# Kernel tuning notes

Measured on AMD Instinct MI355X. Metric: run time of the kernel, lower is better.

Reference implementation:

```python
import jax, jax.numpy as jnp
import numpy as np

D_MODEL = 1024
N_HEADS = 16
WINDOW = 256
CAUSAL = True


def build_sliding_window_mask(T, window_size, causal=True):
    half = window_size // 2
    i = jnp.arange(T)[:, None]
    j = jnp.arange(T)[None, :]
    attend = jnp.abs(i - j) <= half
    if causal:
        attend = attend & (j <= i)
    return jnp.where(attend, 0.0, -jnp.inf).astype(jnp.float32)  # (T, T)


def setup_inputs() -> dict:
    key = jax.random.key(0)
    kx, kq, kk, kv, ko = jax.random.split(key, 5)
    B, T, D = 2, 2048, D_MODEL
    s = 1.0 / np.sqrt(D)
    return {
        "x": jax.random.normal(kx, (B, T, D), jnp.float32),
        "Wq": jax.random.normal(kq, (D, D), jnp.float32) * s,
        "Wk": jax.random.normal(kk, (D, D), jnp.float32) * s,
        "Wv": jax.random.normal(kv, (D, D), jnp.float32) * s,
        "Wo": jax.random.normal(ko, (D, D), jnp.float32) * s,
    }


def reference(x, Wq, Wk, Wv, Wo):
    B, T, D = x.shape
    H = N_HEADS
    dh = D // H
    # torch nn.Linear: y = x @ W.T
    def proj(W):
        return (x @ W.T).reshape(B, T, H, dh).transpose(0, 2, 1, 3)  # (B,H,T,dh)

    q, k, v = proj(Wq), proj(Wk), proj(Wv)
    scale = jnp.sqrt(jnp.asarray(dh, x.dtype))
    scores = jnp.einsum("bhtd,bhsd->bhts", q, k) / scale  # (B,H,T,T)
    mask = build_sliding_window_mask(T, WINDOW, CAUSAL)
    scores = scores + mask[None, None]
    attn = jax.nn.softmax(scores, axis=-1)
    attn = jnp.nan_to_num(attn, nan=0.0)
    out = jnp.einsum("bhts,bhsd->bhtd", attn, v)  # (B,H,T,dh)
    out = out.transpose(0, 2, 1, 3).reshape(B, T, D)
    return out @ Wo.T
```

## Files before the change

kernel.cpp:

```cpp
#include <hip/hip_runtime.h>
#include <hip/hip_bf16.h>

#define B_  2
#define T_  2048
#define D_  1024
#define H_  16
#define DH_ 64
#define M_  (B_ * T_)

typedef short s16x8 __attribute__((ext_vector_type(8)));
typedef float f32x4 __attribute__((ext_vector_type(4)));

__device__ inline float bfu(unsigned short u) {
    union { unsigned int i; float f; } c; c.i = ((unsigned int)u) << 16; return c.f;
}
__device__ inline unsigned short f2bf(float f) {
    union { float f; unsigned int i; } c; c.f = f;
    unsigned int r = c.i + 0x7fffu + ((c.i >> 16) & 1u);
    return (unsigned short)(r >> 16);
}
__device__ inline void stv(float* p, float v) { *p = v; }
__device__ inline void stv(unsigned short* p, float v) { *p = f2bf(v); }

__device__ inline void gload_lds16(const unsigned short* g, unsigned short* l) {
    __builtin_amdgcn_global_load_lds(
        (const __attribute__((address_space(1))) void*)g,
        (__attribute__((address_space(3))) void*)l, 16, 0, 0);
}

__global__ __launch_bounds__(256) void conv_bf16(const float* __restrict__ x,
                                                 const float* __restrict__ Wq,
                                                 const float* __restrict__ Wk,
                                                 const float* __restrict__ Wv,
                                                 const float* __restrict__ Wo,
                                                 unsigned short* __restrict__ dst) {
    const int g = blockIdx.x * 256 + threadIdx.x;
    const float* s; size_t o;
    if (g < (1 << 20)) { s = x; o = (size_t)g; }
    else {
        int gg = g - (1 << 20);
        int w = gg >> 18;
        o = (size_t)(gg & ((1 << 18) - 1));
        s = (w == 0) ? Wq : (w == 1) ? Wk : (w == 2) ? Wv : Wo;
    }
    float4 v = ((const float4*)s)[o];
    ushort4 u;
    u.x = f2bf(v.x); u.y = f2bf(v.y); u.z = f2bf(v.z); u.w = f2bf(v.w);
    ((ushort4*)dst)[g] = u;
}

template <int BM, typename Tout>
__global__ __launch_bounds__(256) void gemm_m97(const unsigned short* __restrict__ A,
                                                const unsigned short* __restrict__ Bw,
                                                Tout* __restrict__ C0,
                                                Tout* __restrict__ C1,
                                                Tout* __restrict__ C2,
                                                int K) {
    constexpr int MI = BM / 32;
    __shared__ unsigned short As[BM * 32];
    __shared__ unsigned short Bs[128 * 32];
    const int tid  = threadIdx.x;
    const int lane = tid & 63;
    const int wave = tid >> 6;
    const int wr = wave >> 1, wc = wave & 1;
    const int bm = blockIdx.y * BM, bn = blockIdx.x * 128;
    const int fr = lane & 15, kg = lane >> 4;
    const int lrow = lane >> 2;
    const int lcol = (lane & 3) * 8;

    f32x4 acc[MI][4];
    #pragma unroll
    for (int mi = 0; mi < MI; ++mi)
        #pragma unroll
        for (int ni = 0; ni < 4; ++ni)
            #pragma unroll
            for (int r = 0; r < 4; ++r) acc[mi][ni][r] = 0.f;

    const unsigned short* ga = A  + (size_t)(bm + wave * 16 + lrow) * K + lcol;
    const unsigned short* gb = Bw + (size_t)(bn + wave * 16 + lrow) * K + lcol;
    unsigned short* la = &As[(wave * 16) * 32];
    unsigned short* lb = &Bs[(wave * 16) * 32];

    for (int k0 = 0; k0 < K; k0 += 32) {
        __syncthreads();
        #pragma unroll
        for (int s = 0; s < BM / 64; ++s)
            gload_lds16(ga + k0 + (size_t)(s * 64) * K, la + s * 64 * 32);
        gload_lds16(gb + k0,                  lb);
        gload_lds16(gb + k0 + (size_t)64 * K, lb + 64 * 32);
        __syncthreads();
        s16x8 af[MI], bfv[4];
        #pragma unroll
        for (int mi = 0; mi < MI; ++mi)
            af[mi] = *(const s16x8*)&As[(wr * (BM / 2) + mi * 16 + fr) * 32 + kg * 8];
        #pragma unroll
        for (int ni = 0; ni < 4; ++ni)
            bfv[ni] = *(const s16x8*)&Bs[(wc * 64 + ni * 16 + fr) * 32 + kg * 8];
        #pragma unroll
        for (int mi = 0; mi < MI; ++mi)
            #pragma unroll
            for (int ni = 0; ni < 4; ++ni)
                acc[mi][ni] = __builtin_amdgcn_mfma_f32_16x16x32_bf16(af[mi], bfv[ni], acc[mi][ni], 0, 0, 0);
    }

    Tout* C = (bn < 1024) ? C0 : (bn < 2048) ? C1 : C2;
    const int nb = bn & 1023;
    #pragma unroll
    for (int mi = 0; mi < MI; ++mi)
        #pragma unroll
        for (int ni = 0; ni < 4; ++ni)
            #pragma unroll
            for (int r = 0; r < 4; ++r) {
                int m = bm + wr * (BM / 2) + mi * 16 + kg * 4 + r;
                int n = nb + wc * 64 + ni * 16 + fr;
                stv(&C[(size_t)m * 1024 + n], acc[mi][ni][r]);
            }
}

__global__ __launch_bounds__(256) void transpose_bh(const unsigned short* __restrict__ src0,
                                                    unsigned short* __restrict__ dst) {
    __shared__ unsigned short sm[64][66];
    const int tid = threadIdx.x;
    const int t0 = blockIdx.x * 64;
    const int bh = blockIdx.y;
    const int b = bh >> 4, h = bh & 15;
    const unsigned short* src = src0 + ((size_t)(b * T_ + t0)) * D_ + h * 64;
    #pragma unroll
    for (int kc = 0; kc < 16; ++kc) {
        int idx = kc * 256 + tid;
        int r = idx >> 6, c = idx & 63;
        sm[r][c] = src[(size_t)r * D_ + c];
    }
    __syncthreads();
    unsigned short* d2 = dst + (size_t)bh * 64 * T_ + t0;
    #pragma unroll
    for (int kc = 0; kc < 16; ++kc) {
        int idx = kc * 256 + tid;
        int d = idx >> 6, tt = idx & 63;
        d2[(size_t)d * T_ + tt] = sm[tt][d];
    }
}

__global__ __launch_bounds__(256) void swa_mfma2(const unsigned short* qb,
                                                 const unsigned short* __restrict__ kb,
                                                 const unsigned short* __restrict__ vt,
                                                 unsigned short* ob) {
    __shared__ unsigned short Ks[192 * 64];
    __shared__ unsigned short Pl[4][16 * 168];
    const int wave = threadIdx.x >> 6;
    const int lane = threadIdx.x & 63;
    const int blk = blockIdx.x;
    const int i0b = (blk & 31) * 64;
    const int bh  = blk >> 5;
    const int h = bh & (H_ - 1), b = bh >> 4;
    const int g = lane >> 4, l15 = lane & 15;

    const size_t rowbase = (size_t)b * T_ * D_ + (size_t)h * DH_;
    const int klo2 = (i0b > 128) ? (i0b - 128) : 0;

    {
        const unsigned short* kg0 = kb + rowbase
            + (size_t)(klo2 + (lane >> 3)) * D_ + (lane & 7) * 8;
        #pragma unroll
        for (int s = 0; s < 6; ++s) {
            const int i = wave * 6 + s;
            gload_lds16(kg0 + (size_t)(i * 8) * D_, &Ks[i * 8 * 64]);
        }
    }

    const int i0  = i0b + wave * 16;
    const int klo = (i0 > 128) ? (i0 - 128) : 0;
    const int koff = klo - klo2;

    unsigned short* Pw = Pl[wave];
    {
        int row = lane >> 2, col = 144 + (lane & 3) * 4;
        *(uint2*)&Pw[row * 168 + col] = make_uint2(0u, 0u);
    }

    const unsigned short* qrow = qb + rowbase + (size_t)(i0 + l15) * D_ + g * 8;
    const s16x8 aq0 = *(const s16x8*)(qrow);
    const s16x8 aq1 = *(const s16x8*)(qrow + 32);

    __syncthreads();

    f32x4 sacc[9];
    #pragma unroll
    for (int t = 0; t < 9; ++t)
        #pragma unroll
        for (int r = 0; r < 4; ++r) sacc[t][r] = 0.f;

    #pragma unroll
    for (int t = 0; t < 9; ++t) {
        const unsigned short* kr = &Ks[(koff + t * 16 + l15) * 64 + g * 8];
        s16x8 b0 = *(const s16x8*)kr;
        s16x8 b1 = *(const s16x8*)(kr + 32);
        sacc[t] = __builtin_amdgcn_mfma_f32_16x16x32_bf16(aq0, b0, sacc[t], 0, 0, 0);
        sacc[t] = __builtin_amdgcn_mfma_f32_16x16x32_bf16(aq1, b1, sacc[t], 0, 0, 0);
    }

    float mrow[4] = {-1e30f, -1e30f, -1e30f, -1e30f};
    #pragma unroll
    for (int t = 0; t < 9; ++t)
        #pragma unroll
        for (int r = 0; r < 4; ++r) {
            const int j  = klo + t * 16 + l15;
            const int iq = i0 + g * 4 + r;
            const bool valid = (j <= iq) && (j + 128 >= iq);
            const float s = valid ? sacc[t][r] * 0.125f : -1e30f;
            sacc[t][r] = s;
            mrow[r] = fmaxf(mrow[r], s);
        }
    #pragma unroll
    for (int r = 0; r < 4; ++r)
        #pragma unroll
        for (int off = 1; off < 16; off <<= 1)
            mrow[r] = fmaxf(mrow[r], __shfl_xor(mrow[r], off));

    float lrow[4] = {0.f, 0.f, 0.f, 0.f};
    #pragma unroll
    for (int t = 0; t < 9; ++t)
        #pragma unroll
        for (int r = 0; r < 4; ++r) {
            const float p = __expf(sacc[t][r] - mrow[r]);
            sacc[t][r] = p;
            lrow[r] += p;
        }
    #pragma unroll
    for (int r = 0; r < 4; ++r) {
        #pragma unroll
        for (int off = 1; off < 16; off <<= 1)
            lrow[r] += __shfl_xor(lrow[r], off);
    }
    float invl[4];
    #pragma unroll
    for (int r = 0; r < 4; ++r) invl[r] = 1.f / lrow[r];

    #pragma unroll
    for (int t = 0; t < 9; ++t)
        #pragma unroll
        for (int r = 0; r < 4; ++r)
            Pw[(g * 4 + r) * 168 + t * 16 + l15] = f2bf(sacc[t][r]);

    f32x4 oacc[4];
    #pragma unroll
    for (int nt = 0; nt < 4; ++nt)
        #pragma unroll
        for (int r = 0; r < 4; ++r) oacc[nt][r] = 0.f;

    const unsigned short* vtb = vt + (size_t)bh * 64 * T_;
    #pragma unroll
    for (int kt = 0; kt < 5; ++kt) {
        const s16x8 ap = *(const s16x8*)&Pw[l15 * 168 + kt * 32 + g * 8];
        #pragma unroll
        for (int nt = 0; nt < 4; ++nt) {
            const unsigned short* vrow = vtb + (size_t)(nt * 16 + l15) * T_ + klo + kt * 32 + g * 8;
            s16x8 bv = *(const s16x8*)vrow;
            oacc[nt] = __builtin_amdgcn_mfma_f32_16x16x32_bf16(ap, bv, oacc[nt], 0, 0, 0);
        }
    }

    #pragma unroll
    for (int nt = 0; nt < 4; ++nt)
        #pragma unroll
        for (int r = 0; r < 4; ++r) {
            const float val = oacc[nt][r] * invl[r];
            ob[rowbase + (size_t)(i0 + g * 4 + r) * D_ + nt * 16 + l15] = f2bf(val);
        }
}

extern "C" void kernel_launch(void* const* d_in, const int* in_sizes, int n_in,
                              void* d_out, int out_size, void* d_ws, size_t ws_size,
                              hipStream_t stream) {
    const float* x  = (const float*)d_in[0];
    const float* Wq = (const float*)d_in[1];
    const float* Wk = (const float*)d_in[2];
    const float* Wv = (const float*)d_in[3];
    const float* Wo = (const float*)d_in[4];

    const size_t MD = (size_t)M_ * D_;
    const size_t WN = (size_t)D_ * D_;

    unsigned short* wsb = (unsigned short*)d_ws;
    unsigned short* xb  = wsb;
    unsigned short* Wqb = xb + MD;
    unsigned short* Wob = Wqb + 3 * WN;
    unsigned short* qb  = Wob + WN;
    unsigned short* vb  = qb + MD;
    unsigned short* vt = (unsigned short*)d_out;
    unsigned short* kb = vt + MD;

    conv_bf16<<<8192, 256, 0, stream>>>(x, Wq, Wk, Wv, Wo, wsb);

    gemm_m97<128, unsigned short><<<dim3(24, M_ / 128), 256, 0, stream>>>(
        xb, Wqb, qb, kb, vb, D_);
    transpose_bh<<<dim3(T_ / 64, B_ * H_), 256, 0, stream>>>(vb, vt);

    swa_mfma2<<<(B_ * H_ * T_) / 64, 256, 0, stream>>>(qb, kb, vt, qb);

    gemm_m97<64, float><<<dim3(8, M_ / 64), 256, 0, stream>>>(
        qb, Wob, (float*)d_out, (float*)d_out, (float*)d_out, D_);
}
```

Baseline: 164.2 us.

## Fuse V transpose into QKV GEMM epilogue and double K-step per sync

The QKV projection GEMM now writes the V slice straight into the per-head transposed layout (b,h,d,t) from its accumulator registers, so the separate transpose kernel and the intermediate V buffer are gone. The GEMM main loop also loads two 32-wide K slices per barrier pair, which halves the number of __syncthreads and doubles the LDS footprint. The transposed stores are 4-element ushort4 writes strided by T, so they may coalesce less well than a dedicated transpose.

Measured after the change: 156.4 us. -4.7%, faster.

```diff
diff --git a/kernel.cpp b/kernel.cpp
--- a/kernel.cpp
+++ b/kernel.cpp
@@ -54,11 +54,11 @@
                                                 const unsigned short* __restrict__ Bw,
                                                 Tout* __restrict__ C0,
                                                 Tout* __restrict__ C1,
-                                                Tout* __restrict__ C2,
+                                                unsigned short* __restrict__ vtr,
                                                 int K) {
     constexpr int MI = BM / 32;
-    __shared__ unsigned short As[BM * 32];
-    __shared__ unsigned short Bs[128 * 32];
+    __shared__ unsigned short As[2 * BM * 32];
+    __shared__ unsigned short Bs[2 * 128 * 32];
     const int tid  = threadIdx.x;
     const int lane = tid & 63;
     const int wave = tid >> 6;
@@ -81,29 +81,52 @@
     unsigned short* la = &As[(wave * 16) * 32];
     unsigned short* lb = &Bs[(wave * 16) * 32];
 
-    for (int k0 = 0; k0 < K; k0 += 32) {
+    for (int k0 = 0; k0 < K; k0 += 64) {
         __syncthreads();
         #pragma unroll
-        for (int s = 0; s < BM / 64; ++s)
-            gload_lds16(ga + k0 + (size_t)(s * 64) * K, la + s * 64 * 32);
-        gload_lds16(gb + k0,                  lb);
-        gload_lds16(gb + k0 + (size_t)64 * K, lb + 64 * 32);
+        for (int hf = 0; hf < 2; ++hf) {
+            #pragma unroll
+            for (int s = 0; s < BM / 64; ++s)
+                gload_lds16(ga + k0 + hf * 32 + (size_t)(s * 64) * K,
+                            la + hf * BM * 32 + s * 64 * 32);
+            gload_lds16(gb + k0 + hf * 32,                  lb + hf * 128 * 32);
+            gload_lds16(gb + k0 + hf * 32 + (size_t)64 * K, lb + hf * 128 * 32 + 64 * 32);
+        }
         __syncthreads();
-        s16x8 af[MI], bfv[4];
+        #pragma unroll
+        for (int hf = 0; hf < 2; ++hf) {
+            s16x8 af[MI], bfv[4];
+            #pragma unroll
+            for (int mi = 0; mi < MI; ++mi)
+                af[mi] = *(const s16x8*)&As[hf * BM * 32 + (wr * (BM / 2) + mi * 16 + fr) * 32 + kg * 8];
+            #pragma unroll
+            for (int ni = 0; ni < 4; ++ni)
+                bfv[ni] = *(const s16x8*)&Bs[hf * 128 * 32 + (wc * 64 + ni * 16 + fr) * 32 + kg * 8];
+            #pragma unroll
+            for (int mi = 0; mi < MI; ++mi)
+                #pragma unroll
+                for (int ni = 0; ni < 4; ++ni)
+                    acc[mi][ni] = __builtin_amdgcn_mfma_f32_16x16x32_bf16(af[mi], bfv[ni], acc[mi][ni], 0, 0, 0);
+        }
+    }
+
+    if (vtr && bn >= 2048) {
         #pragma unroll
         for (int mi = 0; mi < MI; ++mi)
-            af[mi] = *(const s16x8*)&As[(wr * (BM / 2) + mi * 16 + fr) * 32 + kg * 8];
-        #pragma unroll
-        for (int ni = 0; ni < 4; ++ni)
-            bfv[ni] = *(const s16x8*)&Bs[(wc * 64 + ni * 16 + fr) * 32 + kg * 8];
-        #pragma unroll
-        for (int mi = 0; mi < MI; ++mi)
-            #pragma unroll
-            for (int ni = 0; ni < 4; ++ni)
-                acc[mi][ni] = __builtin_amdgcn_mfma_f32_16x16x32_bf16(af[mi], bfv[ni], acc[mi][ni], 0, 0, 0);
-    }
-
-    Tout* C = (bn < 1024) ? C0 : (bn < 2048) ? C1 : C2;
+            #pragma unroll
+            for (int ni = 0; ni < 4; ++ni) {
+                const int nl = (bn - 2048) + wc * 64 + ni * 16 + fr;
+                const int h = nl >> 6, d = nl & 63;
+                const int m0 = bm + wr * (BM / 2) + mi * 16 + kg * 4;
+                const int b = m0 >> 11, t0 = m0 & (T_ - 1);
+                ushort4 u;
+                u.x = f2bf(acc[mi][ni][0]); u.y = f2bf(acc[mi][ni][1]);
+                u.z = f2bf(acc[mi][ni][2]); u.w = f2bf(acc[mi][ni][3]);
+                *(ushort4*)(vtr + ((size_t)(b * H_ + h) * 64 + d) * T_ + t0) = u;
+            }
+        return;
+    }
+    Tout* C = (bn < 1024) ? C0 : C1;
     const int nb = bn & 1023;
     #pragma unroll
     for (int mi = 0; mi < MI; ++mi)
@@ -115,30 +138,6 @@
                 int n = nb + wc * 64 + ni * 16 + fr;
                 stv(&C[(size_t)m * 1024 + n], acc[mi][ni][r]);
             }
-}
-
-__global__ __launch_bounds__(256) void transpose_bh(const unsigned short* __restrict__ src0,
-                                                    unsigned short* __restrict__ dst) {
-    __shared__ unsigned short sm[64][66];
-    const int tid = threadIdx.x;
-    const int t0 = blockIdx.x * 64;
-    const int bh = blockIdx.y;
-    const int b = bh >> 4, h = bh & 15;
-    const unsigned short* src = src0 + ((size_t)(b * T_ + t0)) * D_ + h * 64;
-    #pragma unroll
-    for (int kc = 0; kc < 16; ++kc) {
-        int idx = kc * 256 + tid;
-        int r = idx >> 6, c = idx & 63;
-        sm[r][c] = src[(size_t)r * D_ + c];
-    }
-    __syncthreads();
-    unsigned short* d2 = dst + (size_t)bh * 64 * T_ + t0;
-    #pragma unroll
-    for (int kc = 0; kc < 16; ++kc) {
-        int idx = kc * 256 + tid;
-        int d = idx >> 6, tt = idx & 63;
-        d2[(size_t)d * T_ + tt] = sm[tt][d];
-    }
 }
 
 __global__ __launch_bounds__(256) void swa_mfma2(const unsigned short* qb,
@@ -286,18 +285,16 @@
     unsigned short* Wqb = xb + MD;
     unsigned short* Wob = Wqb + 3 * WN;
     unsigned short* qb  = Wob + WN;
-    unsigned short* vb  = qb + MD;
     unsigned short* vt = (unsigned short*)d_out;
     unsigned short* kb = vt + MD;
 
     conv_bf16<<<8192, 256, 0, stream>>>(x, Wq, Wk, Wv, Wo, wsb);
 
     gemm_m97<128, unsigned short><<<dim3(24, M_ / 128), 256, 0, stream>>>(
-        xb, Wqb, qb, kb, vb, D_);
-    transpose_bh<<<dim3(T_ / 64, B_ * H_), 256, 0, stream>>>(vb, vt);
+        xb, Wqb, qb, kb, vt, D_);
 
     swa_mfma2<<<(B_ * H_ * T_) / 64, 256, 0, stream>>>(qb, kb, vt, qb);
 
     gemm_m97<64, float><<<dim3(8, M_ / 64), 256, 0, stream>>>(
-        qb, Wob, (float*)d_out, (float*)d_out, (float*)d_out, D_);
-}
+        qb, Wob, (float*)d_out, (float*)d_out, nullptr, D_);
+}
```
